# Performance work log

Hardware: AMD Instinct MI355X
Metric: run time of the kernel (lower is better)

## Reference

```python
import jax, jax.numpy as jnp
import numpy as np

B, S, F, K = 64, 1024, 128, 64  # batch, seq(=l), feat(=d), bottleneck k


def setup_inputs() -> dict:
    key = jax.random.key(0)
    ks = jax.random.split(key, 24)
    r = lambda k_, sh, s=0.05: (jax.random.normal(k_, sh, dtype=jnp.float32) * s)
    inp = {
        'f1_norm': jax.random.normal(ks[0], (B, S, F), dtype=jnp.float32),
        'f2_norm': jax.random.normal(ks[1], (B, S, F), dtype=jnp.float32),
        'f3_norm': jax.random.normal(ks[2], (B, S, F), dtype=jnp.float32),
        # AMLP params (Linear(F, 2F))
        'Wi': r(ks[3], (2 * F, F)), 'bi': r(ks[4], (2 * F,)),
        'Wq': r(ks[5], (2 * F, F)), 'bq': r(ks[6], (2 * F,)),
        'Wvp': r(ks[7], (2 * F, F)), 'bvp': r(ks[8], (2 * F,)),
        # affine_{a,v,l}: Linear(l, l, bias=False) -> weight [l, l]
        'Aa': r(ks[9], (S, S)), 'Av': r(ks[10], (S, S)), 'Al': r(ks[11], (S, S)),
        # W_{a,v,t}: Linear(l, k) -> [k, l]
        'Wa': r(ks[12], (K, S)), 'Wv': r(ks[13], (K, S)), 'Wt': r(ks[14], (K, S)),
        # W_c{a,v,t}: Linear(2d, k) -> [k, 2F]
        'Wca': r(ks[15], (K, 2 * F)), 'Wcv': r(ks[16], (K, 2 * F)), 'Wct': r(ks[17], (K, 2 * F)),
        # W_h{a,v,t}: Linear(k, l) -> [l, k]
        'Wha': r(ks[18], (S, K)), 'Whv': r(ks[19], (S, K)), 'Wht': r(ks[20], (S, K)),
    }
    return inp


def _amlp(txt, aud, vis, Wi, bi, Wq, bq, Wvp, bvp):
    f1 = jnp.einsum('bsf,gf->bsg', txt, Wi) + bi  # [B,S,2F]
    f2 = jnp.einsum('bsf,gf->bsg', aud, Wq) + bq
    f3 = jnp.einsum('bsf,gf->bsg', vis, Wvp) + bvp
    n1 = jnp.linalg.norm(f1)
    n2 = jnp.linalg.norm(f2)
    n3 = jnp.linalg.norm(f3)
    # faithful to source: third term is scalar factor3 * norm3 (broadcast)
    exp_out = (n1 / (n1 + n2)) * f1 + (n2 / (n1 + n2)) * f2 + (n3 / (n1 + n2 + n3)) * n3
    b, s, g = exp_out.shape
    z = exp_out.reshape(b, s, g // 2, 2).sum(-1)  # AvgPool1d(2,2) * 2 == pair sum
    # F.normalize default dim=1 (over sequence axis for 3D tensor)
    z = z / jnp.maximum(jnp.linalg.norm(z, axis=1, keepdims=True), 1e-12)
    return z  # [B,S,F]


def reference(f1_norm, f2_norm, f3_norm, Wi, bi, Wq, bq, Wvp, bvp,
              Aa, Av, Al, Wa, Wv, Wt, Wca, Wcv, Wct, Wha, Whv, Wht):
    txt, aud, vis = f1_norm, f2_norm, f3_norm
    G = _amlp(txt, aud, vis, Wi, bi, Wq, bq, Wvp, bvp)  # [B,S,F]

    G_ag = jnp.concatenate([aud, G], axis=-1)  # [B,S,2F]
    G_vg = jnp.concatenate([vis, G], axis=-1)
    G_lg = jnp.concatenate([txt, G], axis=-1)
    scale = np.sqrt(G_ag.shape[-1]).astype(np.float32)  # sqrt(2F); same for all three

    # a_j = affine(G_xg^T); att = x^T @ a_j^T  ==  x^T @ (A @ G_xg)
    AGa = jnp.einsum('ts,bsc->btc', Aa, G_ag)
    C_a = jnp.tanh(jnp.einsum('bsf,bsc->bfc', aud, AGa) / scale)  # [B,F,2F]
    AGv = jnp.einsum('ts,bsc->btc', Av, G_ag)  # NOTE: source bug uses G_ag, not G_vg
    C_v = jnp.tanh(jnp.einsum('bsf,bsc->bfc', vis, AGv) / scale)
    AGl = jnp.einsum('ts,bsc->btc', Al, G_lg)
    C_t = jnp.tanh(jnp.einsum('bsf,bsc->bfc', txt, AGl) / scale)

    H_a = jax.nn.relu(jnp.einsum('bfc,kc->bfk', C_a, Wca) + jnp.einsum('bsf,ks->bfk', aud, Wa))
    H_v = jax.nn.relu(jnp.einsum('bfc,kc->bfk', C_v, Wcv) + jnp.einsum('bsf,ks->bfk', vis, Wv))
    H_t = jax.nn.relu(jnp.einsum('bfc,kc->bfk', C_t, Wct) + jnp.einsum('bsf,ks->bfk', txt, Wt))

    out_a = jnp.einsum('bfk,sk->bsf', H_a, Wha) + aud  # [B,S,F]
    out_v = jnp.einsum('bfk,sk->bsf', H_v, Whv) + vis
    out_t = jnp.einsum('bfk,sk->bsf', H_t, Wht) + txt
    return (out_t, out_a, out_v)
```

## Files before the change

### kernel.cpp

```cpp
#include <hip/hip_runtime.h>
#include <math.h>

constexpr int Bb = 64;
constexpr int Ss = 1024;
constexpr int Ff = 128;
constexpr int G2 = 256;
constexpr int Kk = 64;
constexpr int NE = 1152;

typedef __bf16 bfrag __attribute__((ext_vector_type(8)));
typedef float  facc  __attribute__((ext_vector_type(4)));
typedef short  s8v   __attribute__((ext_vector_type(8)));
typedef short  s4v   __attribute__((ext_vector_type(4)));

__device__ __forceinline__ short f2bfs(float f) {
  union { float f; unsigned u; } v; v.f = f;
  unsigned r = v.u + 0x7FFFu + ((v.u >> 16) & 1u);
  return (short)(r >> 16);
}
__device__ __forceinline__ float bf2fs(short s) {
  union { unsigned u; float f; } v; v.u = ((unsigned)(unsigned short)s) << 16;
  return v.f;
}
__device__ __forceinline__ facc mfma16(bfrag a, bfrag b, facc c) {
  return __builtin_amdgcn_mfma_f32_16x16x32_bf16(a, b, c, 0, 0, 0);
}
__device__ __forceinline__ void gld16(const void* g, void* l) {
  __builtin_amdgcn_global_load_lds(
      (const __attribute__((address_space(1))) void*)g,
      (__attribute__((address_space(3))) void*)l, 16, 0, 0);
}

__global__ void k_transpose(const float* __restrict__ aud, const float* __restrict__ vis,
                            const float* __restrict__ txt, short* __restrict__ xT) {
  __shared__ float tile[64][65];
  int z = blockIdx.z;
  int mod = z >> 6, b = z & 63;
  const float* x = (mod == 0) ? aud : (mod == 1) ? vis : txt;
  int s0 = blockIdx.x * 64, f0 = blockIdx.y * 64;
  int tid = threadIdx.x;
  {
    int fg = tid & 15, sb = tid >> 4;
#pragma unroll
    for (int i = 0; i < 4; ++i) {
      int si = i * 16 + sb;
      float4 v = *(const float4*)(x + ((size_t)b * Ss + s0 + si) * Ff + f0 + fg * 4);
      tile[si][fg * 4 + 0] = v.x;
      tile[si][fg * 4 + 1] = v.y;
      tile[si][fg * 4 + 2] = v.z;
      tile[si][fg * 4 + 3] = v.w;
    }
  }
  __syncthreads();
  short* dst = xT + ((size_t)mod * Bb + b) * Ff * Ss;
  {
    int sg = tid & 15, fb = tid >> 4;
#pragma unroll
    for (int i = 0; i < 4; ++i) {
      int fi = i * 16 + fb;
      s4v v;
      v[0] = f2bfs(tile[sg * 4 + 0][fi]);
      v[1] = f2bfs(tile[sg * 4 + 1][fi]);
      v[2] = f2bfs(tile[sg * 4 + 2][fi]);
      v[3] = f2bfs(tile[sg * 4 + 3][fi]);
      *(s4v*)(dst + (size_t)(f0 + fi) * Ss + s0 + sg * 4) = v;
    }
  }
}

__global__ void k_build_aextT(const float* __restrict__ Aa, const float* __restrict__ Av,
                              const float* __restrict__ Al, const float* __restrict__ Wa,
                              const float* __restrict__ Wv, const float* __restrict__ Wt,
                              short* __restrict__ aextT) {
  __shared__ float tile[64][65];
  int mod = blockIdx.z;
  const float* A = (mod == 0) ? Aa : (mod == 1) ? Av : Al;
  const float* W = (mod == 0) ? Wa : (mod == 1) ? Wv : Wt;
  short* dst = aextT + (size_t)mod * NE * Ss;
  int n0 = blockIdx.x * 64, t0 = blockIdx.y * 64;
  int tid = threadIdx.x;
  if (n0 < Ss) {
    for (int i = 0; i < 16; ++i) {
      int idx = i * 256 + tid;
      int ti = idx >> 6, nj = idx & 63;
      tile[ti][nj] = A[(size_t)(t0 + ti) * Ss + n0 + nj];
    }
    __syncthreads();
    int tg = tid & 15, nb = tid >> 4;
#pragma unroll
    for (int i = 0; i < 4; ++i) {
      int nj = i * 16 + nb;
      s4v v;
      v[0] = f2bfs(tile[tg * 4 + 0][nj]);
      v[1] = f2bfs(tile[tg * 4 + 1][nj]);
      v[2] = f2bfs(tile[tg * 4 + 2][nj]);
      v[3] = f2bfs(tile[tg * 4 + 3][nj]);
      *(s4v*)(dst + (size_t)(n0 + nj) * Ss + t0 + tg * 4) = v;
    }
  } else if (n0 < Ss + Kk) {
    for (int i = 0; i < 16; ++i) {
      int idx = i * 256 + tid;
      int j = idx >> 6, tt = idx & 63;
      dst[(size_t)(n0 + j) * Ss + t0 + tt] = f2bfs(W[(size_t)(n0 - Ss + j) * Ss + t0 + tt]);
    }
  } else {
    for (int i = 0; i < 16; ++i) {
      int idx = i * 256 + tid;
      int j = idx >> 6, tt = idx & 63;
      dst[(size_t)(n0 + j) * Ss + t0 + tt] = 0;
    }
  }
}

__global__ void k_build_w(const float* __restrict__ Wca, const float* __restrict__ Wcv,
                          const float* __restrict__ Wct, const float* __restrict__ Wha,
                          const float* __restrict__ Whv, const float* __restrict__ Wht,
                          const float* __restrict__ Wi, const float* __restrict__ Wq,
                          const float* __restrict__ Wvp,
                          short* __restrict__ wcb, short* __restrict__ whb,
                          short* __restrict__ wbar) {
  int idx = blockIdx.x * 256 + threadIdx.x;
  const int n1 = 3 * Kk * G2;
  const int n2 = n1 + 3 * Ss * Kk;
  if (idx < n1) {
    int mod = idx / (Kk * G2), r = idx - mod * (Kk * G2);
    const float* W = (mod == 0) ? Wca : (mod == 1) ? Wcv : Wct;
    wcb[idx] = f2bfs(W[r]);
  } else if (idx < n2) {
    int j = idx - n1;
    int mod = j / (Ss * Kk), r = j - mod * (Ss * Kk);
    const float* W = (mod == 0) ? Wha : (mod == 1) ? Whv : Wht;
    whb[j] = f2bfs(W[r]);
  } else {
    int j = idx - n2;
    int mod = j / (G2 * Ff), r = j - mod * (G2 * Ff);
    int n = r >> 7, k = r & 127;
    int t = n >> 4, nl = n & 15;
    int c = k >> 5, q = (k >> 3) & 3, e = k & 7;
    const float* W = (mod == 0) ? Wi : (mod == 1) ? Wq : Wvp;
    wbar[mod * G2 * Ff + (((t * 4 + c) * 64 + q * 16 + nl) * 8) + e] = f2bfs(W[r]);
  }
}

__global__ void __launch_bounds__(256, 3) k_amlp(
    const float* __restrict__ txt, const float* __restrict__ aud, const float* __restrict__ vis,
    const float* __restrict__ bi, const float* __restrict__ bq, const float* __restrict__ bvp,
    const short* __restrict__ wbar,
    short* __restrict__ p1, short* __restrict__ p2, float* __restrict__ sumsq) {
  int mod = blockIdx.y;
  const float* x    = (mod == 0) ? txt : (mod == 1) ? aud : vis;
  const float* bias = (mod == 0) ? bi  : (mod == 1) ? bq  : bvp;
  const short* wbm  = wbar + mod * G2 * Ff;
  short* pout = (mod == 0) ? p1 : (mod == 1) ? p2 : nullptr;

  __shared__ float wred[4];
  int tid = threadIdx.x, lane = tid & 63, wave = tid >> 6;
  int quad = lane >> 4, nl = lane & 15;

  bfrag wreg[4][4];
#pragma unroll
  for (int tt = 0; tt < 4; ++tt)
#pragma unroll
    for (int c = 0; c < 4; ++c)
      wreg[tt][c] = *(const bfrag*)(wbm + ((((wave * 4 + tt) * 4 + c) * 64 + lane) * 8));

  float bia[4];
#pragma unroll
  for (int tt = 0; tt < 4; ++tt) bia[tt] = bias[wave * 64 + tt * 16 + nl];

  const float* xblk = x + (size_t)(blockIdx.x * 256) * Ff;
  facc zero = {0.f, 0.f, 0.f, 0.f};
  float sq = 0.f;

  float4 buf[8];
  {
    const float* xrow = xblk + (size_t)nl * Ff;
#pragma unroll
    for (int c = 0; c < 4; ++c) {
      buf[c * 2]     = *(const float4*)(xrow + c * 32 + quad * 8);
      buf[c * 2 + 1] = *(const float4*)(xrow + c * 32 + quad * 8 + 4);
    }
  }

  for (int g = 0; g < 16; ++g) {
    bfrag af[4];
#pragma unroll
    for (int c = 0; c < 4; ++c) {
      float4 a0 = buf[c * 2], a1 = buf[c * 2 + 1];
      af[c][0] = (__bf16)a0.x; af[c][1] = (__bf16)a0.y;
      af[c][2] = (__bf16)a0.z; af[c][3] = (__bf16)a0.w;
      af[c][4] = (__bf16)a1.x; af[c][5] = (__bf16)a1.y;
      af[c][6] = (__bf16)a1.z; af[c][7] = (__bf16)a1.w;
    }
    if (g < 15) {
      const float* xrow = xblk + (size_t)((g + 1) * 16 + nl) * Ff;
#pragma unroll
      for (int c = 0; c < 4; ++c) {
        buf[c * 2]     = *(const float4*)(xrow + c * 32 + quad * 8);
        buf[c * 2 + 1] = *(const float4*)(xrow + c * 32 + quad * 8 + 4);
      }
    }
    facc acc[4];
#pragma unroll
    for (int tt = 0; tt < 4; ++tt) acc[tt] = zero;
#pragma unroll
    for (int c = 0; c < 4; ++c)
#pragma unroll
      for (int tt = 0; tt < 4; ++tt)
        acc[tt] = mfma16(af[c], wreg[tt][c], acc[tt]);

    int drow = blockIdx.x * 256 + g * 16 + quad * 4;
#pragma unroll
    for (int tt = 0; tt < 4; ++tt)
#pragma unroll
      for (int r = 0; r < 4; ++r) {
        float fv = acc[tt][r] + bia[tt];
        sq += fv * fv;
        if (pout) {
          float fo = fv + __shfl_xor(fv, 1, 64);
          if ((lane & 1) == 0)
            pout[(size_t)(drow + r) * Ff + wave * 32 + tt * 8 + (nl >> 1)] = f2bfs(fo);
        }
      }
  }
  for (int off = 32; off > 0; off >>= 1) sq += __shfl_down(sq, off, 64);
  if (lane == 0) wred[wave] = sq;
  __syncthreads();
  if (tid == 0) atomicAdd(&sumsq[mod], wred[0] + wred[1] + wred[2] + wred[3]);
}

__global__ void k_colnorm(const short* __restrict__ p1, const short* __restrict__ p2,
                          const float* __restrict__ sumsq, float* __restrict__ colnsq) {
  float n1 = sqrtf(sumsq[0]), n2 = sqrtf(sumsq[1]), n3 = sqrtf(sumsq[2]);
  float w1 = n1 / (n1 + n2), w2 = n2 / (n1 + n2);
  float tc = 2.f * n3 * n3 / (n1 + n2 + n3);
  int b = blockIdx.x, j = threadIdx.x;
  int s0 = blockIdx.y * 64;
  float a = 0.f;
  for (int s = s0; s < s0 + 64; ++s) {
    size_t off = ((size_t)b * Ss + s) * Ff + j;
    float z = w1 * bf2fs(p1[off]) + w2 * bf2fs(p2[off]) + tc;
    a += z * z;
  }
  atomicAdd(&colnsq[b * Ff + j], a);
}

__global__ void k_gnormT(const short* __restrict__ p1, const short* __restrict__ p2,
                         const float* __restrict__ sumsq, const float* __restrict__ colnsq,
                         short* __restrict__ gT) {
  __shared__ float tile[64][65];
  __shared__ float invcn[64];
  float n1 = sqrtf(sumsq[0]), n2 = sqrtf(sumsq[1]), n3 = sqrtf(sumsq[2]);
  float w1 = n1 / (n1 + n2), w2 = n2 / (n1 + n2);
  float tc = 2.f * n3 * n3 / (n1 + n2 + n3);
  int b = blockIdx.z, s0 = blockIdx.x * 64, f0 = blockIdx.y * 64;
  int tid = threadIdx.x;
  if (tid < 64)
    invcn[tid] = 1.f / fmaxf(sqrtf(colnsq[b * Ff + f0 + tid]), 1e-12f);
  __syncthreads();
  for (int i = 0; i < 16; ++i) {
    int idx = i * 256 + tid;
    int si = idx >> 6, fi = idx & 63;
    size_t off = ((size_t)b * Ss + s0 + si) * Ff + f0 + fi;
    float z = w1 * bf2fs(p1[off]) + w2 * bf2fs(p2[off]) + tc;
    tile[si][fi] = z * invcn[fi];
  }
  __syncthreads();
  short* dst = gT + (size_t)b * Ff * Ss;
  {
    int sg = tid & 15, fb = tid >> 4;
#pragma unroll
    for (int i = 0; i < 4; ++i) {
      int fi = i * 16 + fb;
      s4v v;
      v[0] = f2bfs(tile[sg * 4 + 0][fi]);
      v[1] = f2bfs(tile[sg * 4 + 1][fi]);
      v[2] = f2bfs(tile[sg * 4 + 2][fi]);
      v[3] = f2bfs(tile[sg * 4 + 3][fi]);
      *(s4v*)(dst + (size_t)(f0 + fi) * Ss + s0 + sg * 4) = v;
    }
  }
}

__global__ void __launch_bounds__(256) k_mgemm(const short* __restrict__ xT,
                                               const short* __restrict__ aextT,
                                               short* __restrict__ mxext) {
  int mod = blockIdx.z;
  const short* Ap = xT + (size_t)mod * Bb * Ff * Ss;
  const short* Bp = aextT + (size_t)mod * NE * Ss;
  short* Op = mxext + (size_t)mod * Bb * Ff * NE;
  int M0 = blockIdx.x * 128, N0 = blockIdx.y * 128;
  __shared__ short As[128 * 64];
  __shared__ short Bs[128 * 64];
  int tid = threadIdx.x, lane = tid & 63, wave = tid >> 6;
  int quad = lane >> 4, nl = lane & 15;
  int wm = (wave >> 1) * 64, wn = (wave & 1) * 64;
  facc zero = {0.f, 0.f, 0.f, 0.f};
  facc acc[4][4];
  for (int i = 0; i < 4; ++i) for (int j = 0; j < 4; ++j) acc[i][j] = zero;
  for (int k0 = 0; k0 < Ss; k0 += 64) {
    __syncthreads();
#pragma unroll
    for (int i = 0; i < 4; ++i) {
      int idx = i * 256 + tid;
      int r = idx >> 3, cs = ((idx & 7) ^ (r & 7)) * 8;
      gld16(Ap + (size_t)(M0 + r) * Ss + k0 + cs, As + idx * 8);
      gld16(Bp + (size_t)(N0 + r) * Ss + k0 + cs, Bs + idx * 8);
    }
    __syncthreads();
#pragma unroll
    for (int kc = 0; kc < 2; ++kc) {
      bfrag a[4], bfr[4];
      for (int mt = 0; mt < 4; ++mt) {
        int row = wm + mt * 16 + nl;
        a[mt] = *(const bfrag*)(As + row * 64 + (((kc * 4 + quad) ^ (row & 7)) * 8));
      }
      for (int nt = 0; nt < 4; ++nt) {
        int row = wn + nt * 16 + nl;
        bfr[nt] = *(const bfrag*)(Bs + row * 64 + (((kc * 4 + quad) ^ (row & 7)) * 8));
      }
      for (int mt = 0; mt < 4; ++mt)
        for (int nt = 0; nt < 4; ++nt)
          acc[mt][nt] = mfma16(a[mt], bfr[nt], acc[mt][nt]);
    }
  }
  for (int mt = 0; mt < 4; ++mt)
    for (int nt = 0; nt < 4; ++nt)
      for (int r = 0; r < 4; ++r) {
        int row = M0 + wm + mt * 16 + quad * 4 + r;
        int col = N0 + wn + nt * 16 + nl;
        Op[(size_t)row * NE + col] = f2bfs(acc[mt][nt][r]);
      }
}

__global__ void __launch_bounds__(256) k_chgemm(const short* __restrict__ mxext,
                                                const short* __restrict__ xT,
                                                const short* __restrict__ gT,
                                                const short* __restrict__ wcb,
                                                short* __restrict__ h) {
  int b = blockIdx.x, mod = blockIdx.y, half = blockIdx.z;
  int r0 = half * 64;
  const short* Ap = mxext + ((size_t)mod * Bb + b) * Ff * NE;
  const short* xTb = xT + (size_t)((mod == 2) ? 2 : 0) * Bb * Ff * Ss + (size_t)b * Ff * Ss;
  const short* gTb = gT + (size_t)b * Ff * Ss;
  const short* Wp = wcb + (size_t)mod * Kk * G2;
  short* Hp = h + ((size_t)mod * Bb + b) * Ff * Kk;

  __shared__ short smem[64 * 64 + 256 * 64];
  short* As = smem;
  short* Bs = smem + 64 * 64;

  int tid = threadIdx.x, lane = tid & 63, wave = tid >> 6;
  int quad = lane >> 4, nl = lane & 15;
  int wn = wave * 64;
  facc zero = {0.f, 0.f, 0.f, 0.f};
  facc acc[4][4];
  for (int i = 0; i < 4; ++i) for (int j = 0; j < 4; ++j) acc[i][j] = zero;
  for (int k0 = 0; k0 < Ss; k0 += 64) {
    __syncthreads();
#pragma unroll
    for (int i = 0; i < 2; ++i) {
      int idx = i * 256 + tid;
      int r = idx >> 3, cs = ((idx & 7) ^ (r & 7)) * 8;
      gld16(Ap + (size_t)(r0 + r) * NE + k0 + cs, As + idx * 8);
    }
#pragma unroll
    for (int i = 0; i < 8; ++i) {
      int idx = i * 256 + tid;
      int r = idx >> 3, cs = ((idx & 7) ^ (r & 7)) * 8;
      const short* src = (r < 128) ? (xTb + (size_t)r * Ss) : (gTb + (size_t)(r - 128) * Ss);
      gld16(src + k0 + cs, Bs + idx * 8);
    }
    __syncthreads();
#pragma unroll
    for (int kc = 0; kc < 2; ++kc) {
      bfrag a[4], bfr[4];
      for (int mt = 0; mt < 4; ++mt) {
        int row = mt * 16 + nl;
        a[mt] = *(const bfrag*)(As + row * 64 + (((kc * 4 + quad) ^ (row & 7)) * 8));
      }
      for (int nt = 0; nt < 4; ++nt) {
        int row = wn + nt * 16 + nl;
        bfr[nt] = *(const bfrag*)(Bs + row * 64 + (((kc * 4 + quad) ^ (row & 7)) * 8));
      }
      for (int mt = 0; mt < 4; ++mt)
        for (int nt = 0; nt < 4; ++nt)
          acc[mt][nt] = mfma16(a[mt], bfr[nt], acc[mt][nt]);
    }
  }
  __syncthreads();
  short* Cs = smem;
  for (int mt = 0; mt < 4; ++mt)
    for (int nt = 0; nt < 4; ++nt)
      for (int r = 0; r < 4; ++r) {
        int row = mt * 16 + quad * 4 + r;
        int col = wn + nt * 16 + nl;
        Cs[row * 272 + col] = f2bfs(tanhf(acc[mt][nt][r] * 0.0625f));
      }
  __syncthreads();
  facc hacc[4];
  for (int nt = 0; nt < 4; ++nt) hacc[nt] = zero;
  for (int k0 = 0; k0 < G2; k0 += 32) {
    bfrag ca = *(const bfrag*)(Cs + (wave * 16 + nl) * 272 + k0 + quad * 8);
    for (int nt = 0; nt < 4; ++nt) {
      bfrag wb = *(const bfrag*)(Wp + (size_t)(nt * 16 + nl) * G2 + k0 + quad * 8);
      hacc[nt] = mfma16(ca, wb, hacc[nt]);
    }
  }
  for (int nt = 0; nt < 4; ++nt)
    for (int r = 0; r < 4; ++r) {
      int row = r0 + wave * 16 + quad * 4 + r;
      int col = nt * 16 + nl;
      float v = hacc[nt][r] + bf2fs(Ap[(size_t)row * NE + Ss + col]);
      Hp[(size_t)row * Kk + col] = f2bfs(fmaxf(v, 0.f));
    }
}

__global__ void k_outgemm(const short* __restrict__ whb, const short* __restrict__ h,
                          const float* __restrict__ txt, const float* __restrict__ aud,
                          const float* __restrict__ vis, float* __restrict__ outp) {
  int s0 = blockIdx.x * 128, b = blockIdx.y, mod = blockIdx.z;
  const short* Wp = whb + (size_t)mod * Ss * Kk;
  const short* Hp = h + ((size_t)mod * Bb + b) * Ff * Kk;
  const float* xres = ((mod == 0) ? aud : (mod == 1) ? vis : txt) + (size_t)b * Ss * Ff;
  int slot = (mod == 0) ? 1 : (mod == 1) ? 2 : 0;
  float* Op = outp + ((size_t)slot * Bb + b) * Ss * Ff;
  int tid = threadIdx.x, lane = tid & 63, wave = tid >> 6;
  int quad = lane >> 4, nl = lane & 15;
  int wm = (wave >> 1) * 64, wn = (wave & 1) * 64;
  facc zero = {0.f, 0.f, 0.f, 0.f};
  facc acc[4][4];
  for (int i = 0; i < 4; ++i) for (int j = 0; j < 4; ++j) acc[i][j] = zero;
  for (int k0 = 0; k0 < Kk; k0 += 32) {
    bfrag a[4], bfr[4];
    for (int mt = 0; mt < 4; ++mt)
      a[mt] = *(const bfrag*)(Wp + (size_t)(s0 + wm + mt * 16 + nl) * Kk + k0 + quad * 8);
    for (int nt = 0; nt < 4; ++nt)
      bfr[nt] = *(const bfrag*)(Hp + (size_t)(wn + nt * 16 + nl) * Kk + k0 + quad * 8);
    for (int mt = 0; mt < 4; ++mt)
      for (int nt = 0; nt < 4; ++nt)
        acc[mt][nt] = mfma16(a[mt], bfr[nt], acc[mt][nt]);
  }
  for (int mt = 0; mt < 4; ++mt)
    for (int nt = 0; nt < 4; ++nt)
      for (int r = 0; r < 4; ++r) {
        int srow = s0 + wm + mt * 16 + quad * 4 + r;
        int col = wn + nt * 16 + nl;
        size_t o = (size_t)srow * Ff + col;
        Op[o] = acc[mt][nt][r] + xres[o];
      }
}

extern "C" void kernel_launch(void* const* d_in, const int* in_sizes, int n_in,
                              void* d_out, int out_size, void* d_ws, size_t ws_size,
                              hipStream_t stream) {
  const float* txt = (const float*)d_in[0];
  const float* aud = (const float*)d_in[1];
  const float* vis = (const float*)d_in[2];
  const float* Wi  = (const float*)d_in[3];
  const float* bi  = (const float*)d_in[4];
  const float* Wq  = (const float*)d_in[5];
  const float* bq  = (const float*)d_in[6];
  const float* Wvp = (const float*)d_in[7];
  const float* bvp = (const float*)d_in[8];
  const float* Aa  = (const float*)d_in[9];
  const float* Av  = (const float*)d_in[10];
  const float* Al  = (const float*)d_in[11];
  const float* Wa  = (const float*)d_in[12];
  const float* Wv  = (const float*)d_in[13];
  const float* Wt  = (const float*)d_in[14];
  const float* Wca = (const float*)d_in[15];
  const float* Wcv = (const float*)d_in[16];
  const float* Wct = (const float*)d_in[17];
  const float* Wha = (const float*)d_in[18];
  const float* Whv = (const float*)d_in[19];
  const float* Wht = (const float*)d_in[20];

  char* w = (char*)d_ws;
  float* sumsq  = (float*)w;
  float* colnsq = (float*)(w + 256);
  size_t off = 65536;
  short* xT    = (short*)(w + off); off += (size_t)3 * Bb * Ff * Ss * 2;
  short* aextT = (short*)(w + off); off += (size_t)3 * NE * Ss * 2;
  short* gT    = (short*)(w + off); off += (size_t)Bb * Ff * Ss * 2;
  short* mx    = (short*)(w + off);
  short* p1    = mx;
  short* p2    = mx + (size_t)Bb * Ss * Ff;
  off += (size_t)3 * Bb * Ff * NE * 2;
  short* h     = (short*)(w + off); off += (size_t)3 * Bb * Ff * Kk * 2;
  short* wcb   = (short*)(w + off); off += (size_t)3 * Kk * G2 * 2;
  short* whb   = (short*)(w + off); off += (size_t)3 * Ss * Kk * 2;
  short* wbar  = (short*)(w + off); off += (size_t)3 * G2 * Ff * 2;

  hipMemsetAsync(d_ws, 0, 65536, stream);
  k_transpose<<<dim3(16, 2, 192), 256, 0, stream>>>(aud, vis, txt, xT);
  k_build_aextT<<<dim3(NE / 64, 16, 3), 256, 0, stream>>>(Aa, Av, Al, Wa, Wv, Wt, aextT);
  k_build_w<<<(3 * Kk * G2 + 3 * Ss * Kk + 3 * G2 * Ff) / 256, 256, 0, stream>>>(
      Wca, Wcv, Wct, Wha, Whv, Wht, Wi, Wq, Wvp, wcb, whb, wbar);
  k_amlp<<<dim3(Bb * Ss / 256, 3), 256, 0, stream>>>(txt, aud, vis, bi, bq, bvp,
                                                     wbar, p1, p2, sumsq);
  k_colnorm<<<dim3(Bb, 16), 128, 0, stream>>>(p1, p2, sumsq, colnsq);
  k_gnormT<<<dim3(16, 2, Bb), 256, 0, stream>>>(p1, p2, sumsq, colnsq, gT);
  k_mgemm<<<dim3(Bb * Ff / 128, NE / 128, 3), 256, 0, stream>>>(xT, aextT, mx);
  k_chgemm<<<dim3(Bb, 3, 2), 256, 0, stream>>>(mx, xT, gT, wcb, h);
  k_outgemm<<<dim3(Ss / 128, Bb, 3), 256, 0, stream>>>(whb, h, txt, aud, vis, (float*)d_out);
}
```

Before: 446.6 us.

## Move x^T·W_s term from mgemm into chgemm and vectorize colnorm

Removes the 128 extra N columns (Wa/Wv/Wt plus padding) from the big mgemm, shrinking its output and work by about 11%, and instead computes the x^T W_s bottleneck term inside chgemm with extra MFMAs that read xT and a new bf16 weight buffer directly from global memory. Also vectorizes the A-matrix load in build_aextT, rewrites colnorm to use 8-wide loads and a shared-memory reduction, and swizzles the mgemm block order along M. The chgemm grid is small (384 blocks), so adding uncached global fragment loads to its inner loop may lengthen it.

```diff
diff --git a/kernel.cpp b/kernel.cpp
--- a/kernel.cpp
+++ b/kernel.cpp
@@ -6,7 +6,7 @@
 constexpr int Ff = 128;
 constexpr int G2 = 256;
 constexpr int Kk = 64;
-constexpr int NE = 1152;
+constexpr int NA = 1024;
 
 typedef __bf16 bfrag __attribute__((ext_vector_type(8)));
 typedef float  facc  __attribute__((ext_vector_type(4)));
@@ -69,23 +69,27 @@
 }
 
 __global__ void k_build_aextT(const float* __restrict__ Aa, const float* __restrict__ Av,
-                              const float* __restrict__ Al, const float* __restrict__ Wa,
-                              const float* __restrict__ Wv, const float* __restrict__ Wt,
-                              short* __restrict__ aextT) {
+                              const float* __restrict__ Al, short* __restrict__ aextT) {
   __shared__ float tile[64][65];
   int mod = blockIdx.z;
   const float* A = (mod == 0) ? Aa : (mod == 1) ? Av : Al;
-  const float* W = (mod == 0) ? Wa : (mod == 1) ? Wv : Wt;
-  short* dst = aextT + (size_t)mod * NE * Ss;
+  short* dst = aextT + (size_t)mod * NA * Ss;
   int n0 = blockIdx.x * 64, t0 = blockIdx.y * 64;
   int tid = threadIdx.x;
-  if (n0 < Ss) {
-    for (int i = 0; i < 16; ++i) {
-      int idx = i * 256 + tid;
-      int ti = idx >> 6, nj = idx & 63;
-      tile[ti][nj] = A[(size_t)(t0 + ti) * Ss + n0 + nj];
-    }
-    __syncthreads();
+  {
+    int fg = tid & 15, sb = tid >> 4;
+#pragma unroll
+    for (int i = 0; i < 4; ++i) {
+      int ti = i * 16 + sb;
+      float4 v = *(const float4*)(A + (size_t)(t0 + ti) * Ss + n0 + fg * 4);
+      tile[ti][fg * 4 + 0] = v.x;
+      tile[ti][fg * 4 + 1] = v.y;
+      tile[ti][fg * 4 + 2] = v.z;
+      tile[ti][fg * 4 + 3] = v.w;
+    }
+  }
+  __syncthreads();
+  {
     int tg = tid & 15, nb = tid >> 4;
 #pragma unroll
     for (int i = 0; i < 4; ++i) {
@@ -97,18 +101,6 @@
       v[3] = f2bfs(tile[tg * 4 + 3][nj]);
       *(s4v*)(dst + (size_t)(n0 + nj) * Ss + t0 + tg * 4) = v;
     }
-  } else if (n0 < Ss + Kk) {
-    for (int i = 0; i < 16; ++i) {
-      int idx = i * 256 + tid;
-      int j = idx >> 6, tt = idx & 63;
-      dst[(size_t)(n0 + j) * Ss + t0 + tt] = f2bfs(W[(size_t)(n0 - Ss + j) * Ss + t0 + tt]);
-    }
-  } else {
-    for (int i = 0; i < 16; ++i) {
-      int idx = i * 256 + tid;
-      int j = idx >> 6, tt = idx & 63;
-      dst[(size_t)(n0 + j) * Ss + t0 + tt] = 0;
-    }
   }
 }
 
@@ -116,12 +108,14 @@
                           const float* __restrict__ Wct, const float* __restrict__ Wha,
                           const float* __restrict__ Whv, const float* __restrict__ Wht,
                           const float* __restrict__ Wi, const float* __restrict__ Wq,
-                          const float* __restrict__ Wvp,
+                          const float* __restrict__ Wvp, const float* __restrict__ Wa,
+                          const float* __restrict__ Wv, const float* __restrict__ Wt,
                           short* __restrict__ wcb, short* __restrict__ whb,
-                          short* __restrict__ wbar) {
+                          short* __restrict__ wbar, short* __restrict__ wsb) {
   int idx = blockIdx.x * 256 + threadIdx.x;
   const int n1 = 3 * Kk * G2;
   const int n2 = n1 + 3 * Ss * Kk;
+  const int n3 = n2 + 3 * G2 * Ff;
   if (idx < n1) {
     int mod = idx / (Kk * G2), r = idx - mod * (Kk * G2);
     const float* W = (mod == 0) ? Wca : (mod == 1) ? Wcv : Wct;
@@ -131,7 +125,7 @@
     int mod = j / (Ss * Kk), r = j - mod * (Ss * Kk);
     const float* W = (mod == 0) ? Wha : (mod == 1) ? Whv : Wht;
     whb[j] = f2bfs(W[r]);
-  } else {
+  } else if (idx < n3) {
     int j = idx - n2;
     int mod = j / (G2 * Ff), r = j - mod * (G2 * Ff);
     int n = r >> 7, k = r & 127;
@@ -139,6 +133,11 @@
     int c = k >> 5, q = (k >> 3) & 3, e = k & 7;
     const float* W = (mod == 0) ? Wi : (mod == 1) ? Wq : Wvp;
     wbar[mod * G2 * Ff + (((t * 4 + c) * 64 + q * 16 + nl) * 8) + e] = f2bfs(W[r]);
+  } else {
+    int j = idx - n3;
+    int mod = j / (Kk * Ss), r = j - mod * (Kk * Ss);
+    const float* W = (mod == 0) ? Wa : (mod == 1) ? Wv : Wt;
+    wsb[j] = f2bfs(W[r]);
   }
 }
 
@@ -231,18 +230,33 @@
 
 __global__ void k_colnorm(const short* __restrict__ p1, const short* __restrict__ p2,
                           const float* __restrict__ sumsq, float* __restrict__ colnsq) {
+  __shared__ float part[16][128];
   float n1 = sqrtf(sumsq[0]), n2 = sqrtf(sumsq[1]), n3 = sqrtf(sumsq[2]);
   float w1 = n1 / (n1 + n2), w2 = n2 / (n1 + n2);
   float tc = 2.f * n3 * n3 / (n1 + n2 + n3);
-  int b = blockIdx.x, j = threadIdx.x;
-  int s0 = blockIdx.y * 64;
-  float a = 0.f;
-  for (int s = s0; s < s0 + 64; ++s) {
-    size_t off = ((size_t)b * Ss + s) * Ff + j;
-    float z = w1 * bf2fs(p1[off]) + w2 * bf2fs(p2[off]) + tc;
-    a += z * z;
-  }
-  atomicAdd(&colnsq[b * Ff + j], a);
+  int b = blockIdx.x, s0 = blockIdx.y * 128;
+  int tid = threadIdx.x, fi = (tid & 15) * 8, sl = tid >> 4;
+  float a[8];
+#pragma unroll
+  for (int j = 0; j < 8; ++j) a[j] = 0.f;
+  for (int st = 0; st < 8; ++st) {
+    size_t off = ((size_t)b * Ss + s0 + st * 16 + sl) * Ff + fi;
+    s8v v1 = *(const s8v*)(p1 + off);
+    s8v v2 = *(const s8v*)(p2 + off);
+#pragma unroll
+    for (int j = 0; j < 8; ++j) {
+      float z = w1 * bf2fs(v1[j]) + w2 * bf2fs(v2[j]) + tc;
+      a[j] += z * z;
+    }
+  }
+#pragma unroll
+  for (int j = 0; j < 8; ++j) part[sl][fi + j] = a[j];
+  __syncthreads();
+  if (tid < 128) {
+    float s = 0.f;
+    for (int i = 0; i < 16; ++i) s += part[i][tid];
+    atomicAdd(&colnsq[b * Ff + tid], s);
+  }
 }
 
 __global__ void k_gnormT(const short* __restrict__ p1, const short* __restrict__ p2,
@@ -284,12 +298,14 @@
 
 __global__ void __launch_bounds__(256) k_mgemm(const short* __restrict__ xT,
                                                const short* __restrict__ aextT,
-                                               short* __restrict__ mxext) {
+                                               short* __restrict__ mx) {
   int mod = blockIdx.z;
   const short* Ap = xT + (size_t)mod * Bb * Ff * Ss;
-  const short* Bp = aextT + (size_t)mod * NE * Ss;
-  short* Op = mxext + (size_t)mod * Bb * Ff * NE;
-  int M0 = blockIdx.x * 128, N0 = blockIdx.y * 128;
+  const short* Bp = aextT + (size_t)mod * NA * Ss;
+  short* Op = mx + (size_t)mod * Bb * Ff * NA;
+  int bx = blockIdx.x;
+  int swzx = (bx & 7) * 8 + (bx >> 3);
+  int M0 = swzx * 128, N0 = blockIdx.y * 128;
   __shared__ short As[128 * 64];
   __shared__ short Bs[128 * 64];
   int tid = threadIdx.x, lane = tid & 63, wave = tid >> 6;
@@ -329,24 +345,27 @@
       for (int r = 0; r < 4; ++r) {
         int row = M0 + wm + mt * 16 + quad * 4 + r;
         int col = N0 + wn + nt * 16 + nl;
-        Op[(size_t)row * NE + col] = f2bfs(acc[mt][nt][r]);
-      }
-}
-
-__global__ void __launch_bounds__(256) k_chgemm(const short* __restrict__ mxext,
+        Op[(size_t)row * NA + col] = f2bfs(acc[mt][nt][r]);
+      }
+}
+
+__global__ void __launch_bounds__(256) k_chgemm(const short* __restrict__ mx,
                                                 const short* __restrict__ xT,
                                                 const short* __restrict__ gT,
                                                 const short* __restrict__ wcb,
+                                                const short* __restrict__ wsb,
                                                 short* __restrict__ h) {
   int b = blockIdx.x, mod = blockIdx.y, half = blockIdx.z;
   int r0 = half * 64;
-  const short* Ap = mxext + ((size_t)mod * Bb + b) * Ff * NE;
+  const short* Ap = mx + ((size_t)mod * Bb + b) * Ff * NA;
   const short* xTb = xT + (size_t)((mod == 2) ? 2 : 0) * Bb * Ff * Ss + (size_t)b * Ff * Ss;
+  const short* xTm = xT + (size_t)mod * Bb * Ff * Ss + (size_t)b * Ff * Ss;
   const short* gTb = gT + (size_t)b * Ff * Ss;
-  const short* Wp = wcb + (size_t)mod * Kk * G2;
+  const short* Wp  = wcb + (size_t)mod * Kk * G2;
+  const short* Wsp = wsb + (size_t)mod * Kk * Ss;
   short* Hp = h + ((size_t)mod * Bb + b) * Ff * Kk;
 
-  __shared__ short smem[64 * 64 + 256 * 64];
+  __shared__ short smem[64 * 272 + 64 * 72];
   short* As = smem;
   short* Bs = smem + 64 * 64;
 
@@ -355,14 +374,16 @@
   int wn = wave * 64;
   facc zero = {0.f, 0.f, 0.f, 0.f};
   facc acc[4][4];
+  facc t2a[4];
   for (int i = 0; i < 4; ++i) for (int j = 0; j < 4; ++j) acc[i][j] = zero;
+  for (int i = 0; i < 4; ++i) t2a[i] = zero;
   for (int k0 = 0; k0 < Ss; k0 += 64) {
     __syncthreads();
 #pragma unroll
     for (int i = 0; i < 2; ++i) {
       int idx = i * 256 + tid;
       int r = idx >> 3, cs = ((idx & 7) ^ (r & 7)) * 8;
-      gld16(Ap + (size_t)(r0 + r) * NE + k0 + cs, As + idx * 8);
+      gld16(Ap + (size_t)(r0 + r) * NA + k0 + cs, As + idx * 8);
     }
 #pragma unroll
     for (int i = 0; i < 8; ++i) {
@@ -374,7 +395,7 @@
     __syncthreads();
 #pragma unroll
     for (int kc = 0; kc < 2; ++kc) {
-      bfrag a[4], bfr[4];
+      bfrag a[4], bfr[4], xa[4], wf;
       for (int mt = 0; mt < 4; ++mt) {
         int row = mt * 16 + nl;
         a[mt] = *(const bfrag*)(As + row * 64 + (((kc * 4 + quad) ^ (row & 7)) * 8));
@@ -384,12 +405,18 @@
         bfr[nt] = *(const bfrag*)(Bs + row * 64 + (((kc * 4 + quad) ^ (row & 7)) * 8));
       }
       for (int mt = 0; mt < 4; ++mt)
+        xa[mt] = *(const bfrag*)(xTm + (size_t)(r0 + mt * 16 + nl) * Ss + k0 + kc * 32 + quad * 8);
+      wf = *(const bfrag*)(Wsp + (size_t)(wave * 16 + nl) * Ss + k0 + kc * 32 + quad * 8);
+      for (int mt = 0; mt < 4; ++mt)
         for (int nt = 0; nt < 4; ++nt)
           acc[mt][nt] = mfma16(a[mt], bfr[nt], acc[mt][nt]);
-    }
-  }
-  __syncthreads();
-  short* Cs = smem;
+      for (int mt = 0; mt < 4; ++mt)
+        t2a[mt] = mfma16(xa[mt], wf, t2a[mt]);
+    }
+  }
+  __syncthreads();
+  short* Cs  = smem;
+  short* T2s = smem + 64 * 272;
   for (int mt = 0; mt < 4; ++mt)
     for (int nt = 0; nt < 4; ++nt)
       for (int r = 0; r < 4; ++r) {
@@ -397,6 +424,9 @@
         int col = wn + nt * 16 + nl;
         Cs[row * 272 + col] = f2bfs(tanhf(acc[mt][nt][r] * 0.0625f));
       }
+  for (int mt = 0; mt < 4; ++mt)
+    for (int r = 0; r < 4; ++r)
+      T2s[(mt * 16 + quad * 4 + r) * 72 + wave * 16 + nl] = f2bfs(t2a[mt][r]);
   __syncthreads();
   facc hacc[4];
   for (int nt = 0; nt < 4; ++nt) hacc[nt] = zero;
@@ -409,10 +439,10 @@
   }
   for (int nt = 0; nt < 4; ++nt)
     for (int r = 0; r < 4; ++r) {
-      int row = r0 + wave * 16 + quad * 4 + r;
+      int lrow = wave * 16 + quad * 4 + r;
       int col = nt * 16 + nl;
-      float v = hacc[nt][r] + bf2fs(Ap[(size_t)row * NE + Ss + col]);
-      Hp[(size_t)row * Kk + col] = f2bfs(fmaxf(v, 0.f));
+      float v = hacc[nt][r] + bf2fs(T2s[lrow * 72 + col]);
+      Hp[(size_t)(r0 + lrow) * Kk + col] = f2bfs(fmaxf(v, 0.f));
     }
 }
 
@@ -481,27 +511,28 @@
   float* colnsq = (float*)(w + 256);
   size_t off = 65536;
   short* xT    = (short*)(w + off); off += (size_t)3 * Bb * Ff * Ss * 2;
-  short* aextT = (short*)(w + off); off += (size_t)3 * NE * Ss * 2;
+  short* aextT = (short*)(w + off); off += (size_t)3 * NA * Ss * 2;
   short* gT    = (short*)(w + off); off += (size_t)Bb * Ff * Ss * 2;
   short* mx    = (short*)(w + off);
   short* p1    = mx;
   short* p2    = mx + (size_t)Bb * Ss * Ff;
-  off += (size_t)3 * Bb * Ff * NE * 2;
+  off += (size_t)3 * Bb * Ff * NA * 2;
   short* h     = (short*)(w + off); off += (size_t)3 * Bb * Ff * Kk * 2;
   short* wcb   = (short*)(w + off); off += (size_t)3 * Kk * G2 * 2;
   short* whb   = (short*)(w + off); off += (size_t)3 * Ss * Kk * 2;
   short* wbar  = (short*)(w + off); off += (size_t)3 * G2 * Ff * 2;
+  short* wsb   = (short*)(w + off); off += (size_t)3 * Kk * Ss * 2;
 
   hipMemsetAsync(d_ws, 0, 65536, stream);
   k_transpose<<<dim3(16, 2, 192), 256, 0, stream>>>(aud, vis, txt, xT);
-  k_build_aextT<<<dim3(NE / 64, 16, 3), 256, 0, stream>>>(Aa, Av, Al, Wa, Wv, Wt, aextT);
-  k_build_w<<<(3 * Kk * G2 + 3 * Ss * Kk + 3 * G2 * Ff) / 256, 256, 0, stream>>>(
-      Wca, Wcv, Wct, Wha, Whv, Wht, Wi, Wq, Wvp, wcb, whb, wbar);
+  k_build_aextT<<<dim3(16, 16, 3), 256, 0, stream>>>(Aa, Av, Al, aextT);
+  k_build_w<<<(3 * Kk * G2 + 3 * Ss * Kk + 3 * G2 * Ff + 3 * Kk * Ss) / 256, 256, 0, stream>>>(
+      Wca, Wcv, Wct, Wha, Whv, Wht, Wi, Wq, Wvp, Wa, Wv, Wt, wcb, whb, wbar, wsb);
   k_amlp<<<dim3(Bb * Ss / 256, 3), 256, 0, stream>>>(txt, aud, vis, bi, bq, bvp,
                                                      wbar, p1, p2, sumsq);
-  k_colnorm<<<dim3(Bb, 16), 128, 0, stream>>>(p1, p2, sumsq, colnsq);
+  k_colnorm<<<dim3(Bb, 8), 256, 0, stream>>>(p1, p2, sumsq, colnsq);
   k_gnormT<<<dim3(16, 2, Bb), 256, 0, stream>>>(p1, p2, sumsq, colnsq, gT);
-  k_mgemm<<<dim3(Bb * Ff / 128, NE / 128, 3), 256, 0, stream>>>(xT, aextT, mx);
-  k_chgemm<<<dim3(Bb, 3, 2), 256, 0, stream>>>(mx, xT, gT, wcb, h);
+  k_mgemm<<<dim3(Bb * Ff / 128, NA / 128, 3), 256, 0, stream>>>(xT, aextT, mx);
+  k_chgemm<<<dim3(Bb, 3, 2), 256, 0, stream>>>(mx, xT, gT, wcb, wsb, h);
   k_outgemm<<<dim3(Ss / 128, Bb, 3), 256, 0, stream>>>(whb, h, txt, aud, vis, (float*)d_out);
 }
```

New measurement: 466.3 us. 4.4% more time.
